# Optimization experiments

Hardware: AMD Instinct MI355X
Metric: run time of the kernel (lower is better)

## Reference

```python
import jax, jax.numpy as jnp
import numpy as np

B, N, M, K = 4, 16384, 16384, 16   # batch, points, centers, neighbors
C, O, G = 64, 64, 8                # in_planes, out_planes, group


def setup_inputs() -> dict:
    key = jax.random.key(0)
    ks = jax.random.split(key, 16)
    r = lambda i, sh, s=1.0: jax.random.normal(ks[i], sh, jnp.float32) * s
    return dict(
        center_pos=r(0, (B, M, 3)),
        center_fea=r(1, (B, C, M)),
        pos=r(2, (B, N, 3)),
        fea=r(3, (B, C, N)),
        idx=jax.random.randint(ks[4], (B, M, K), 0, N, jnp.int32),
        # linear q/k/v
        Wq=r(5, (C, O), 0.05), bq=jnp.zeros((O,), jnp.float32),
        Wk=r(6, (C, O), 0.05), bk=jnp.zeros((O,), jnp.float32),
        Wv=r(7, (C, O), 0.05), bv=jnp.zeros((O,), jnp.float32),
        # center_pos_encode: conv1x1(3->O, no bias) + folded BN (scale,shift) + relu + conv1x1(O->O)
        cpe_w1=r(8, (3, O), 0.05), cpe_s=jnp.ones((O,), jnp.float32), cpe_b=jnp.zeros((O,), jnp.float32),
        cpe_w2=r(9, (O, O), 0.05), cpe_b2=jnp.zeros((O,), jnp.float32),
        # pos_encode (Conv2d 1x1 == per-point linear)
        pe_w1=r(10, (3, O), 0.05), pe_s=jnp.ones((O,), jnp.float32), pe_b=jnp.zeros((O,), jnp.float32),
        pe_w2=r(11, (O, O), 0.05), pe_b2=jnp.zeros((O,), jnp.float32),
        # weight_encode (O -> G)
        we_w1=r(12, (O, G), 0.05), we_s=jnp.ones((G,), jnp.float32), we_b=jnp.zeros((G,), jnp.float32),
        we_w2=r(13, (G, G), 0.05), we_b2=jnp.zeros((G,), jnp.float32),
    )


def _mlp2(x, w1, s, b, w2, b2):
    # conv1x1(no bias) -> inference BatchNorm folded to (scale, shift) -> ReLU -> conv1x1(+bias)
    h = jax.nn.relu(x @ w1 * s + b)
    return h @ w2 + b2


def reference(center_pos, center_fea, pos, fea, idx,
              Wq, bq, Wk, bk, Wv, bv,
              cpe_w1, cpe_s, cpe_b, cpe_w2, cpe_b2,
              pe_w1, pe_s, pe_b, pe_w2, pe_b2,
              we_w1, we_s, we_b, we_w2, we_b2):
    x_q = center_fea.transpose(0, 2, 1) @ Wq + bq        # [B,M,O]
    ft = fea.transpose(0, 2, 1)                          # [B,N,C]
    x_k = ft @ Wk + bk                                   # [B,N,O]
    x_v = ft @ Wv + bv                                   # [B,N,O]

    gather = jax.vmap(lambda a, i: a[i])                 # per-batch irregular gather
    nk = gather(x_k, idx)                                # [B,M,K,O]
    nv = gather(x_v, idx)                                # [B,M,K,O]
    npos = gather(pos, idx) - center_pos[:, :, None, :]  # [B,M,K,3] relative coords

    cpr = _mlp2(center_pos, cpe_w1, cpe_s, cpe_b, cpe_w2, cpe_b2)  # [B,M,O]
    pr = _mlp2(npos, pe_w1, pe_s, pe_b, pe_w2, pe_b2)              # [B,M,K,O]

    r_qk = nk - x_q[:, :, None, :] + cpr[:, :, None, :]  # [B,M,K,O]
    v = nv + pr                                          # [B,M,K,O]

    w = _mlp2(r_qk, we_w1, we_s, we_b, we_w2, we_b2)     # [B,M,K,G]
    w = jax.nn.softmax(w, axis=2)                        # softmax over neighbors

    v = v.reshape(B, M, K, G, O // G)
    out = jnp.einsum('bmkgi,bmkg->bmgi', v, w).reshape(B, M, O)
    return out.transpose(0, 2, 1)                        # [B,O,M]
```

## Files before the change

kernel.cpp:

```cpp
#include <hip/hip_runtime.h>
#include <hip/hip_bf16.h>

typedef unsigned short u16;
typedef __attribute__((ext_vector_type(8))) __bf16 bf8v;
typedef __attribute__((ext_vector_type(4))) float f32x4;
typedef __attribute__((ext_vector_type(4))) unsigned uint4v;

#define B_ 4
#define N_ 16384
#define M_ 16384
#define K_ 16
#define C_ 64
#define O_ 64
#define G_ 8

__device__ __forceinline__ float bf2f(u16 x){
  union { unsigned u; float f; } v; v.u = ((unsigned)x) << 16; return v.f;
}
__device__ __forceinline__ u16 f2bf(float f){
  union { float f; unsigned u; } v; v.f = f;
  unsigned u = v.u;
  return (u16)((u + 0x7FFFu + ((u >> 16) & 1u)) >> 16);
}
union pk2 { unsigned u; _Float16 h[2]; };
__device__ __forceinline__ unsigned packh(float a, float b){
  pk2 p; p.h[0] = (_Float16)a; p.h[1] = (_Float16)b; return p.u;
}

__global__ __launch_bounds__(256) void setup_kernel(
    const float* __restrict__ Wq, const float* __restrict__ bq,
    const float* __restrict__ cpe_w2, const float* __restrict__ cpe_b2,
    const float* __restrict__ we_w1,
    u16* __restrict__ bw, float* __restrict__ cinit)
{
  __shared__ float sWe[512];
  int tid = threadIdx.x;
  for (int e = tid; e < 512; e += 256) sWe[e] = we_w1[e];
  __syncthreads();
  int k = tid >> 1, g0 = (tid & 1)*4;
  const float* brow = (k < 64) ? (cpe_w2 + k*64) : (Wq + (k-64)*64);
  float sgn = (k < 64) ? 1.f : -1.f;
  float aw[4] = {0.f,0.f,0.f,0.f};
  for (int o = 0; o < 64; o++){
    float bo = brow[o]*sgn;
    #pragma unroll
    for (int gg=0; gg<4; gg++) aw[gg] += bo * sWe[o*8 + g0+gg];
  }
  #pragma unroll
  for (int gg=0; gg<4; gg++) bw[(g0+gg)*136 + k] = f2bf(aw[gg]);
  for (int e = tid; e < 2176; e += 256){
    int r = e / 136, cc = e % 136;
    if (r >= 8 || cc >= 128) bw[e] = 0;
  }
  if (tid < 8){
    float s = 0.f;
    for (int o = 0; o < 64; o++) s += (cpe_b2[o] - bq[o]) * sWe[o*8 + tid];
    cinit[tid] = s;
  }
}

__global__ __launch_bounds__(256) void pre_kernel(
    const float* __restrict__ center_pos, const float* __restrict__ center_fea,
    const float* __restrict__ fea,
    const float* __restrict__ Wk, const float* __restrict__ bk,
    const float* __restrict__ Wv, const float* __restrict__ bv,
    const float* __restrict__ cpe_w1, const float* __restrict__ cpe_s, const float* __restrict__ cpe_b,
    const u16* __restrict__ bw, const float* __restrict__ cinit,
    u16* __restrict__ xk, u16* __restrict__ xv, float* __restrict__ qw)
{
  __shared__ u16 sWT[128*72];
  __shared__ u16 sA[64*72];
  __shared__ u16 sOut[64*136];
  __shared__ float sMisc[256];
  int tid = threadIdx.x;
  int l = tid & 63, w = tid >> 6, c = l & 15, q = l >> 4;
  int blk = blockIdx.x;

  if (blk < 1024){
    int P0 = blk * 64; int b = P0 >> 14; int n0 = P0 & (N_-1);
    const float* fb = fea + (long)b*C_*N_;
    #pragma unroll
    for (int pp = 0; pp < 4; pp++){
      int k = pp*16 + (tid >> 4);
      int nf = (tid & 15)*4;
      f32x4 v = *(const f32x4*)&fb[(long)k*N_ + n0 + nf];
      sA[(nf+0)*72+k] = f2bf(v[0]); sA[(nf+1)*72+k] = f2bf(v[1]);
      sA[(nf+2)*72+k] = f2bf(v[2]); sA[(nf+3)*72+k] = f2bf(v[3]);
    }
    for (int e = tid; e < 8192; e += 256){
      int k = e >> 7, col = e & 127;
      float v = (col < 64) ? Wk[k*64 + col] : Wv[k*64 + (col-64)];
      sWT[col*72 + k] = f2bf(v);
    }
    if (tid < 128) sMisc[tid] = (tid < 64) ? bk[tid] : bv[tid-64];
    __syncthreads();

    bf8v af0 = *(const bf8v*)&sA[(w*16+c)*72 + q*8];
    bf8v af1 = *(const bf8v*)&sA[(w*16+c)*72 + 32 + q*8];

    f32x4 acc[8];
    #pragma unroll
    for (int t = 0; t < 8; t++){
      float bias = sMisc[16*t + c];
      f32x4 a_ = {bias, bias, bias, bias};
      bf8v b0 = *(const bf8v*)&sWT[(16*t + c)*72 + q*8];
      bf8v b1 = *(const bf8v*)&sWT[(16*t + c)*72 + 32 + q*8];
      a_ = __builtin_amdgcn_mfma_f32_16x16x32_bf16(af0, b0, a_, 0,0,0);
      a_ = __builtin_amdgcn_mfma_f32_16x16x32_bf16(af1, b1, a_, 0,0,0);
      acc[t] = a_;
    }
    #pragma unroll
    for (int t = 0; t < 8; t++)
      #pragma unroll
      for (int r = 0; r < 4; r++)
        sOut[(w*16 + q*4 + r)*136 + 16*t + c] = f2bf(acc[t][r]);
    __syncthreads();

    #pragma unroll
    for (int rep = 0; rep < 4; rep++){
      int chunk = rep*256 + tid;
      int pt = chunk >> 4, c8i = chunk & 15;
      uint4v val = *(const uint4v*)&sOut[pt*136 + c8i*8];
      int col8 = c8i*8;
      long row = (long)P0 + pt;
      if (col8 < 64) *(uint4v*)(xk + row*64 + col8)      = val;
      else           *(uint4v*)(xv + row*64 + (col8-64)) = val;
    }
  } else {
    int P0 = (blk - 1024) * 64; int b = P0 >> 14; int m0 = P0 & (M_-1);
    const float* cfb = center_fea + (long)b*C_*M_;
    float* sQ = (float*)sOut;
    #pragma unroll
    for (int pp = 0; pp < 4; pp++){
      int k = pp*16 + (tid >> 4);
      int nf = (tid & 15)*4;
      f32x4 v = *(const f32x4*)&cfb[(long)k*M_ + m0 + nf];
      sA[(nf+0)*72+k] = f2bf(v[0]); sA[(nf+1)*72+k] = f2bf(v[1]);
      sA[(nf+2)*72+k] = f2bf(v[2]); sA[(nf+3)*72+k] = f2bf(v[3]);
    }
    for (int e = tid; e < 2176; e += 256) sWT[e] = bw[e];
    if (tid < 64){
      float sc = cpe_s[tid];
      sMisc[tid]     = cpe_w1[tid]*sc;
      sMisc[64+tid]  = cpe_w1[64+tid]*sc;
      sMisc[128+tid] = cpe_w1[128+tid]*sc;
      sMisc[192+tid] = cpe_b[tid];
    }
    long c3 = (long)(P0 + w*16 + c)*3;
    float cp0 = center_pos[c3], cp1 = center_pos[c3+1], cp2 = center_pos[c3+2];
    __syncthreads();

    bf8v ah[2];
    #pragma unroll
    for (int ks = 0; ks < 2; ks++){
      union { bf8v v; u16 sv[8]; } ua;
      #pragma unroll
      for (int j = 0; j < 8; j++){
        int h = ks*32 + q*8 + j;
        float hv = cp0*sMisc[h] + cp1*sMisc[64+h] + cp2*sMisc[128+h] + sMisc[192+h];
        ua.sv[j] = f2bf(fmaxf(hv, 0.f));
      }
      ah[ks] = ua.v;
    }
    bf8v acf0 = *(const bf8v*)&sA[(w*16+c)*72 + q*8];
    bf8v acf1 = *(const bf8v*)&sA[(w*16+c)*72 + 32 + q*8];

    float ci = (c < 8) ? cinit[c] : 0.f;
    f32x4 aq = {ci, ci, ci, ci};
    {
      bf8v b0 = *(const bf8v*)&sWT[c*136 + q*8];
      bf8v b1 = *(const bf8v*)&sWT[c*136 + 32 + q*8];
      bf8v b2 = *(const bf8v*)&sWT[c*136 + 64 + q*8];
      bf8v b3 = *(const bf8v*)&sWT[c*136 + 96 + q*8];
      aq = __builtin_amdgcn_mfma_f32_16x16x32_bf16(ah[0], b0, aq, 0,0,0);
      aq = __builtin_amdgcn_mfma_f32_16x16x32_bf16(ah[1], b1, aq, 0,0,0);
      aq = __builtin_amdgcn_mfma_f32_16x16x32_bf16(acf0,  b2, aq, 0,0,0);
      aq = __builtin_amdgcn_mfma_f32_16x16x32_bf16(acf1,  b3, aq, 0,0,0);
    }
    __syncthreads();
    if (c < 8){
      #pragma unroll
      for (int r = 0; r < 4; r++) sQ[(w*16 + q*4 + r)*8 + c] = aq[r];
    }
    __syncthreads();
    for (int e = tid; e < 512; e += 256)
      qw[(long)P0*8 + e] = sQ[e];
  }
}

__global__ __launch_bounds__(256) void attn_kernel(
    const float* __restrict__ center_pos, const float* __restrict__ pos,
    const int* __restrict__ idx,
    const float* __restrict__ pe_w1, const float* __restrict__ pe_s, const float* __restrict__ pe_b,
    const float* __restrict__ pe_w2, const float* __restrict__ pe_b2,
    const float* __restrict__ we_w1, const float* __restrict__ we_s, const float* __restrict__ we_b,
    const float* __restrict__ we_w2, const float* __restrict__ we_b2,
    const u16* __restrict__ xk, const u16* __restrict__ xv, const float* __restrict__ qw,
    float* __restrict__ out)
{
  int tid = threadIdx.x;
  __shared__ float s_w1f[192], s_pb[64], s_pb2[64], s_ww2[64];
  __shared__ float s_ws8[8], s_wb8[8], s_wb28[8];
  __shared__ u16  s_stage[64*72 + 16*72];
  __shared__ u16  s_vt[4*2*16*72];
  __shared__ float s_tile[32*66];

  if (tid < 64){
    float sc = pe_s[tid];
    s_w1f[tid]     = pe_w1[tid]*sc;
    s_w1f[64+tid]  = pe_w1[64+tid]*sc;
    s_w1f[128+tid] = pe_w1[128+tid]*sc;
    s_pb[tid]  = pe_b[tid];
    s_pb2[tid] = pe_b2[tid];
    s_ww2[tid] = we_w2[tid];
  }
  if (tid >= 64 && tid < 72){
    int g = tid-64;
    s_ws8[g]=we_s[g]; s_wb8[g]=we_b[g]; s_wb28[g]=we_b2[g];
  }
  #pragma unroll
  for (int pp = 0; pp < 4; pp++){
    int row = pp*16 + (tid >> 4);
    int colf = (tid & 15)*4;
    f32x4 v = *(const f32x4*)&pe_w2[row*64 + colf];
    s_stage[(colf+0)*72+row] = f2bf(v[0]); s_stage[(colf+1)*72+row] = f2bf(v[1]);
    s_stage[(colf+2)*72+row] = f2bf(v[2]); s_stage[(colf+3)*72+row] = f2bf(v[3]);
  }
  u16* s2 = s_stage + 64*72;
  for (int e = tid; e < 512; e += 256){
    int k = e >> 3, cc = e & 7;
    s2[cc*72 + k] = f2bf(we_w1[e]);
  }
  for (int e = tid; e < 576; e += 256) s2[576 + e] = 0;
  __syncthreads();

  int w = tid >> 6, l = tid & 63, c = l & 15, q = l >> 4, c8 = c & 7, qb = l & 48;

  bf8v pw2f[4][2], ww1f[2];
  #pragma unroll
  for (int t = 0; t < 4; t++){
    pw2f[t][0] = *(const bf8v*)&s_stage[(t*16+c)*72 + q*8];
    pw2f[t][1] = *(const bf8v*)&s_stage[(t*16+c)*72 + 32 + q*8];
  }
  ww1f[0] = *(const bf8v*)&s2[c*72 + q*8];
  ww1f[1] = *(const bf8v*)&s2[c*72 + 32 + q*8];

  float ws_c = s_ws8[c8], wb_c = s_wb8[c8], wb2_c = s_wb28[c8];
  float w2col[8];
  #pragma unroll
  for (int g = 0; g < 8; g++) w2col[g] = s_ww2[g*8 + c8];
  float pb2t[4];
  #pragma unroll
  for (int t = 0; t < 4; t++) pb2t[t] = s_pb2[t*16 + c];

  int pbase = blockIdx.x * 32;
  int b = pbase >> 14;
  long xkb = (long)b * N_ * 64;
  u16* vt0 = s_vt + w*(2*16*72);
  u16* vt1 = vt0 + 16*72;
  int ch = c >> 3;

  int pb0 = pbase + w*8;
  int iv0 = idx[(long)pb0*16 + c];
  int iv1 = idx[(long)(pb0+1)*16 + c];
  float qp0 = qw[(long)pb0*8 + c8];
  float qp1 = qw[(long)(pb0+1)*8 + c8];
  long c30 = (long)pb0*3, c31 = (long)(pb0+1)*3;
  float cpA0 = center_pos[c30], cpA1 = center_pos[c30+1], cpA2 = center_pos[c30+2];
  float cpB0 = center_pos[c31], cpB1 = center_pos[c31+1], cpB2 = center_pos[c31+2];

  #pragma unroll 1
  for (int i = 0; i < 4; i++){
    long prA = ((long)b*N_ + iv0)*3, prB = ((long)b*N_ + iv1)*3;
    float pxA = pos[prA], pyA = pos[prA+1], pzA = pos[prA+2];
    float pxB = pos[prB], pyB = pos[prB+1], pzB = pos[prB+2];
    const u16* kr0 = xk + xkb + (long)iv0*64;
    const u16* kr1 = xk + xkb + (long)iv1*64;
    bf8v ka00 = *(const bf8v*)(kr0 + q*8),  ka01 = *(const bf8v*)(kr0 + 32 + q*8);
    bf8v ka10 = *(const bf8v*)(kr1 + q*8),  ka11 = *(const bf8v*)(kr1 + 32 + q*8);
    const u16* vr0 = xv + xkb + (long)iv0*64;
    const u16* vr1 = xv + xkb + (long)iv1*64;
    uint4v va00 = *(const uint4v*)(vr0 + q*8), va01 = *(const uint4v*)(vr0 + 32 + q*8);
    uint4v va10 = *(const uint4v*)(vr1 + q*8), va11 = *(const uint4v*)(vr1 + 32 + q*8);

    int p2 = pb0 + ((i < 3) ? 2*i + 2 : 2*i);
    int p3 = p2 + 1;
    int ivn0 = idx[(long)p2*16 + c];
    int ivn1 = idx[(long)p3*16 + c];
    float qpn0 = qw[(long)p2*8 + c8];
    float qpn1 = qw[(long)p3*8 + c8];
    long c3n0 = (long)p2*3, c3n1 = (long)p3*3;
    float cpnA0 = center_pos[c3n0], cpnA1 = center_pos[c3n0+1], cpnA2 = center_pos[c3n0+2];
    float cpnB0 = center_pos[c3n1], cpnB1 = center_pos[c3n1+1], cpnB2 = center_pos[c3n1+2];

    *(uint4v*)&vt0[c*72 + q*8]      = va00;
    *(uint4v*)&vt0[c*72 + 32 + q*8] = va01;
    *(uint4v*)&vt1[c*72 + q*8]      = va10;
    *(uint4v*)&vt1[c*72 + 32 + q*8] = va11;

    float npA0 = pxA - cpA0, npA1 = pyA - cpA1, npA2 = pzA - cpA2;
    float npB0 = pxB - cpB0, npB1 = pyB - cpB1, npB2 = pzB - cpB2;
    bf8v h1A[2], h1B[2];
    #pragma unroll
    for (int ks = 0; ks < 2; ks++){
      union { bf8v v; u16 s[8]; } ha, hb;
      #pragma unroll
      for (int j = 0; j < 8; j++){
        int o = ks*32 + q*8 + j;
        float w1 = s_w1f[o], w2 = s_w1f[64+o], w3 = s_w1f[128+o], bb = s_pb[o];
        ha.s[j] = f2bf(fmaxf(npA0*w1 + npA1*w2 + npA2*w3 + bb, 0.f));
        hb.s[j] = f2bf(fmaxf(npB0*w1 + npB1*w2 + npB2*w3 + bb, 0.f));
      }
      h1A[ks] = ha.v; h1B[ks] = hb.v;
    }

    f32x4 h2a0 = {qp0, qp0, qp0, qp0};
    f32x4 h2a1 = {qp1, qp1, qp1, qp1};
    h2a0 = __builtin_amdgcn_mfma_f32_16x16x32_bf16(ka00, ww1f[0], h2a0, 0,0,0);
    h2a1 = __builtin_amdgcn_mfma_f32_16x16x32_bf16(ka10, ww1f[0], h2a1, 0,0,0);
    h2a0 = __builtin_amdgcn_mfma_f32_16x16x32_bf16(ka01, ww1f[1], h2a0, 0,0,0);
    h2a1 = __builtin_amdgcn_mfma_f32_16x16x32_bf16(ka11, ww1f[1], h2a1, 0,0,0);

    float h2r0[4], h2r1[4];
    #pragma unroll
    for (int r = 0; r < 4; r++){
      h2r0[r] = fmaxf(h2a0[r]*ws_c + wb_c, 0.f);
      h2r1[r] = fmaxf(h2a1[r]*ws_c + wb_c, 0.f);
    }
    unsigned hp00 = packh(h2r0[0], h2r0[1]), hp01 = packh(h2r0[2], h2r0[3]);
    unsigned hp10 = packh(h2r1[0], h2r1[1]), hp11 = packh(h2r1[2], h2r1[3]);
    float wl0[4] = {wb2_c, wb2_c, wb2_c, wb2_c};
    float wl1[4] = {wb2_c, wb2_c, wb2_c, wb2_c};
    #pragma unroll
    for (int g = 0; g < 8; g++){
      float wg = w2col[g];
      pk2 a0; a0.u = (unsigned)__shfl((int)hp00, qb | g, 64);
      pk2 a1; a1.u = (unsigned)__shfl((int)hp01, qb | g, 64);
      pk2 b0; b0.u = (unsigned)__shfl((int)hp10, qb | g, 64);
      pk2 b1; b1.u = (unsigned)__shfl((int)hp11, qb | g, 64);
      wl0[0] += (float)a0.h[0]*wg; wl0[1] += (float)a0.h[1]*wg;
      wl0[2] += (float)a1.h[0]*wg; wl0[3] += (float)a1.h[1]*wg;
      wl1[0] += (float)b0.h[0]*wg; wl1[1] += (float)b0.h[1]*wg;
      wl1[2] += (float)b1.h[0]*wg; wl1[3] += (float)b1.h[1]*wg;
    }
    float e0[4], e1[4];
    #pragma unroll
    for (int r = 0; r < 4; r++){
      e0[r] = exp2f(wl0[r]*1.44269504f);
      e1[r] = exp2f(wl1[r]*1.44269504f);
    }
    float sm0 = e0[0]+e0[1]+e0[2]+e0[3];
    float sm1 = e1[0]+e1[1]+e1[2]+e1[3];
    sm0 += __shfl_xor(sm0, 16, 64); sm1 += __shfl_xor(sm1, 16, 64);
    sm0 += __shfl_xor(sm0, 32, 64); sm1 += __shfl_xor(sm1, 32, 64);
    float rn0 = 1.0f/sm0, rn1 = 1.0f/sm1;
    #pragma unroll
    for (int r = 0; r < 4; r++){ e0[r] *= rn0; e1[r] *= rn1; }
    unsigned ep00 = packh(e0[0], e0[1]), ep01 = packh(e0[2], e0[3]);
    unsigned ep10 = packh(e1[0], e1[1]), ep11 = packh(e1[2], e1[3]);

    float ov0[4], ov1[4];
    #pragma unroll
    for (int t = 0; t < 4; t++){
      f32x4 z0 = {0.f,0.f,0.f,0.f}, z1 = {0.f,0.f,0.f,0.f};
      z0 = __builtin_amdgcn_mfma_f32_16x16x32_bf16(h1A[0], pw2f[t][0], z0, 0,0,0);
      z1 = __builtin_amdgcn_mfma_f32_16x16x32_bf16(h1B[0], pw2f[t][0], z1, 0,0,0);
      z0 = __builtin_amdgcn_mfma_f32_16x16x32_bf16(h1A[1], pw2f[t][1], z0, 0,0,0);
      z1 = __builtin_amdgcn_mfma_f32_16x16x32_bf16(h1B[1], pw2f[t][1], z1, 0,0,0);
      int src = qb | (t*2 + ch);
      pk2 wA0; wA0.u = (unsigned)__shfl((int)ep00, src, 64);
      pk2 wA1; wA1.u = (unsigned)__shfl((int)ep01, src, 64);
      pk2 wB0; wB0.u = (unsigned)__shfl((int)ep10, src, 64);
      pk2 wB1; wB1.u = (unsigned)__shfl((int)ep11, src, 64);
      float a = 0.f, bacc = 0.f;
      a += (z0[0] + bf2f(vt0[(q*4+0)*72 + t*16 + c])) * (float)wA0.h[0];
      a += (z0[1] + bf2f(vt0[(q*4+1)*72 + t*16 + c])) * (float)wA0.h[1];
      a += (z0[2] + bf2f(vt0[(q*4+2)*72 + t*16 + c])) * (float)wA1.h[0];
      a += (z0[3] + bf2f(vt0[(q*4+3)*72 + t*16 + c])) * (float)wA1.h[1];
      bacc += (z1[0] + bf2f(vt1[(q*4+0)*72 + t*16 + c])) * (float)wB0.h[0];
      bacc += (z1[1] + bf2f(vt1[(q*4+1)*72 + t*16 + c])) * (float)wB0.h[1];
      bacc += (z1[2] + bf2f(vt1[(q*4+2)*72 + t*16 + c])) * (float)wB1.h[0];
      bacc += (z1[3] + bf2f(vt1[(q*4+3)*72 + t*16 + c])) * (float)wB1.h[1];
      ov0[t] = a; ov1[t] = bacc;
    }
    #pragma unroll
    for (int t = 0; t < 4; t++){
      ov0[t] += __shfl_xor(ov0[t], 16, 64);
      ov1[t] += __shfl_xor(ov1[t], 16, 64);
      ov0[t] += __shfl_xor(ov0[t], 32, 64);
      ov1[t] += __shfl_xor(ov1[t], 32, 64);
      ov0[t] += pb2t[t]; ov1[t] += pb2t[t];
    }
    float s0 = ov0[0], s1 = ov1[0];
    s0 = (q==1) ? ov0[1] : s0;  s1 = (q==1) ? ov1[1] : s1;
    s0 = (q==2) ? ov0[2] : s0;  s1 = (q==2) ? ov1[2] : s1;
    s0 = (q==3) ? ov0[3] : s0;  s1 = (q==3) ? ov1[3] : s1;
    s_tile[(w*8 + 2*i + 0)*66 + l] = s0;
    s_tile[(w*8 + 2*i + 1)*66 + l] = s1;

    iv0 = ivn0; iv1 = ivn1; qp0 = qpn0; qp1 = qpn1;
    cpA0 = cpnA0; cpA1 = cpnA1; cpA2 = cpnA2;
    cpB0 = cpnB0; cpB1 = cpnB1; cpB2 = cpnB2;
  }
  __syncthreads();

  int o0 = tid >> 5, pt = tid & 31;
  int m0 = pbase & (M_-1);
  long outb = ((long)b*64) * M_ + m0 + pt;
  #pragma unroll
  for (int ii = 0; ii < 8; ii++){
    int o = o0*8 + ii;
    out[outb + (long)o*M_] = s_tile[pt*66 + o];
  }
}

extern "C" void kernel_launch(void* const* d_in, const int* in_sizes, int n_in,
                              void* d_out, int out_size, void* d_ws, size_t ws_size,
                              hipStream_t stream) {
  const float* center_pos = (const float*)d_in[0];
  const float* center_fea = (const float*)d_in[1];
  const float* pos        = (const float*)d_in[2];
  const float* fea        = (const float*)d_in[3];
  const int*   idx        = (const int*)d_in[4];
  const float* Wq = (const float*)d_in[5];   const float* bq = (const float*)d_in[6];
  const float* Wk = (const float*)d_in[7];   const float* bk = (const float*)d_in[8];
  const float* Wv = (const float*)d_in[9];   const float* bv = (const float*)d_in[10];
  const float* cpe_w1 = (const float*)d_in[11]; const float* cpe_s = (const float*)d_in[12];
  const float* cpe_b  = (const float*)d_in[13]; const float* cpe_w2 = (const float*)d_in[14];
  const float* cpe_b2 = (const float*)d_in[15];
  const float* pe_w1 = (const float*)d_in[16]; const float* pe_s = (const float*)d_in[17];
  const float* pe_b  = (const float*)d_in[18]; const float* pe_w2 = (const float*)d_in[19];
  const float* pe_b2 = (const float*)d_in[20];
  const float* we_w1 = (const float*)d_in[21]; const float* we_s = (const float*)d_in[22];
  const float* we_b  = (const float*)d_in[23]; const float* we_w2 = (const float*)d_in[24];
  const float* we_b2 = (const float*)d_in[25];

  const size_t SZ = (size_t)B_*N_*64;
  u16* xk = (u16*)d_ws;
  u16* xv = xk + SZ;
  float* qwp = (float*)(xv + SZ);
  u16* bwp = (u16*)(qwp + (size_t)B_*M_*8);
  float* cinitp = (float*)(bwp + 2176);
  float* outp = (float*)d_out;

  hipLaunchKernelGGL(setup_kernel, dim3(1), dim3(256), 0, stream,
      Wq, bq, cpe_w2, cpe_b2, we_w1, bwp, cinitp);
  hipLaunchKernelGGL(pre_kernel, dim3(2048), dim3(256), 0, stream,
      center_pos, center_fea, fea, Wk, bk, Wv, bv,
      cpe_w1, cpe_s, cpe_b, bwp, cinitp, xk, xv, qwp);
  hipLaunchKernelGGL(attn_kernel, dim3(2048), dim3(256), 0, stream,
      center_pos, pos, idx, pe_w1, pe_s, pe_b, pe_w2, pe_b2,
      we_w1, we_s, we_b, we_w2, we_b2, xk, xv, qwp, outp);
}
```

Measured before the change: 224.7 us.

## Prepack K/V weights in setup, persist pre blocks, restructure attention per-point loop

```diff
diff --git a/kernel.cpp b/kernel.cpp
--- a/kernel.cpp
+++ b/kernel.cpp
@@ -31,23 +31,29 @@
     const float* __restrict__ Wq, const float* __restrict__ bq,
     const float* __restrict__ cpe_w2, const float* __restrict__ cpe_b2,
     const float* __restrict__ we_w1,
-    u16* __restrict__ bw, float* __restrict__ cinit)
+    const float* __restrict__ Wk, const float* __restrict__ bk,
+    const float* __restrict__ Wv, const float* __restrict__ bv,
+    const float* __restrict__ cpe_w1, const float* __restrict__ cpe_s, const float* __restrict__ cpe_b,
+    u16* __restrict__ bw, float* __restrict__ cinit,
+    u16* __restrict__ wkv, float* __restrict__ bias, float* __restrict__ cpe)
 {
   __shared__ float sWe[512];
   int tid = threadIdx.x;
   for (int e = tid; e < 512; e += 256) sWe[e] = we_w1[e];
   __syncthreads();
-  int k = tid >> 1, g0 = (tid & 1)*4;
-  const float* brow = (k < 64) ? (cpe_w2 + k*64) : (Wq + (k-64)*64);
-  float sgn = (k < 64) ? 1.f : -1.f;
-  float aw[4] = {0.f,0.f,0.f,0.f};
-  for (int o = 0; o < 64; o++){
-    float bo = brow[o]*sgn;
+  {
+    int k = tid >> 1, g0 = (tid & 1)*4;
+    const float* brow = (k < 64) ? (cpe_w2 + k*64) : (Wq + (k-64)*64);
+    float sgn = (k < 64) ? 1.f : -1.f;
+    float aw[4] = {0.f,0.f,0.f,0.f};
+    for (int o = 0; o < 64; o++){
+      float bo = brow[o]*sgn;
+      #pragma unroll
+      for (int gg=0; gg<4; gg++) aw[gg] += bo * sWe[o*8 + g0+gg];
+    }
     #pragma unroll
-    for (int gg=0; gg<4; gg++) aw[gg] += bo * sWe[o*8 + g0+gg];
-  }
-  #pragma unroll
-  for (int gg=0; gg<4; gg++) bw[(g0+gg)*136 + k] = f2bf(aw[gg]);
+    for (int gg=0; gg<4; gg++) bw[(g0+gg)*136 + k] = f2bf(aw[gg]);
+  }
   for (int e = tid; e < 2176; e += 256){
     int r = e / 136, cc = e % 136;
     if (r >= 8 || cc >= 128) bw[e] = 0;
@@ -57,15 +63,27 @@
     for (int o = 0; o < 64; o++) s += (cpe_b2[o] - bq[o]) * sWe[o*8 + tid];
     cinit[tid] = s;
   }
+  for (int e = tid; e < 9216; e += 256){
+    int col = e / 72, k = e - col*72;
+    float v = 0.f;
+    if (k < 64) v = (col < 64) ? Wk[k*64 + col] : Wv[k*64 + (col-64)];
+    wkv[e] = f2bf(v);
+  }
+  if (tid < 128) bias[tid] = (tid < 64) ? bk[tid] : bv[tid-64];
+  if (tid < 64){
+    float sc = cpe_s[tid];
+    cpe[tid]      = cpe_w1[tid]*sc;
+    cpe[64+tid]   = cpe_w1[64+tid]*sc;
+    cpe[128+tid]  = cpe_w1[128+tid]*sc;
+    cpe[192+tid]  = cpe_b[tid];
+  }
 }
 
 __global__ __launch_bounds__(256) void pre_kernel(
     const float* __restrict__ center_pos, const float* __restrict__ center_fea,
     const float* __restrict__ fea,
-    const float* __restrict__ Wk, const float* __restrict__ bk,
-    const float* __restrict__ Wv, const float* __restrict__ bv,
-    const float* __restrict__ cpe_w1, const float* __restrict__ cpe_s, const float* __restrict__ cpe_b,
     const u16* __restrict__ bw, const float* __restrict__ cinit,
+    const u16* __restrict__ wkv, const float* __restrict__ bias, const float* __restrict__ cpe,
     u16* __restrict__ xk, u16* __restrict__ xv, float* __restrict__ qw)
 {
   __shared__ u16 sWT[128*72];
@@ -76,115 +94,118 @@
   int l = tid & 63, w = tid >> 6, c = l & 15, q = l >> 4;
   int blk = blockIdx.x;
 
-  if (blk < 1024){
-    int P0 = blk * 64; int b = P0 >> 14; int n0 = P0 & (N_-1);
+  if (blk < 256){
+    int P0 = blk * 256; int b = P0 >> 14; int n00 = P0 & (N_-1);
     const float* fb = fea + (long)b*C_*N_;
-    #pragma unroll
-    for (int pp = 0; pp < 4; pp++){
-      int k = pp*16 + (tid >> 4);
-      int nf = (tid & 15)*4;
-      f32x4 v = *(const f32x4*)&fb[(long)k*N_ + n0 + nf];
-      sA[(nf+0)*72+k] = f2bf(v[0]); sA[(nf+1)*72+k] = f2bf(v[1]);
-      sA[(nf+2)*72+k] = f2bf(v[2]); sA[(nf+3)*72+k] = f2bf(v[3]);
-    }
-    for (int e = tid; e < 8192; e += 256){
-      int k = e >> 7, col = e & 127;
-      float v = (col < 64) ? Wk[k*64 + col] : Wv[k*64 + (col-64)];
-      sWT[col*72 + k] = f2bf(v);
-    }
-    if (tid < 128) sMisc[tid] = (tid < 64) ? bk[tid] : bv[tid-64];
-    __syncthreads();
-
-    bf8v af0 = *(const bf8v*)&sA[(w*16+c)*72 + q*8];
-    bf8v af1 = *(const bf8v*)&sA[(w*16+c)*72 + 32 + q*8];
-
-    f32x4 acc[8];
-    #pragma unroll
-    for (int t = 0; t < 8; t++){
-      float bias = sMisc[16*t + c];
-      f32x4 a_ = {bias, bias, bias, bias};
-      bf8v b0 = *(const bf8v*)&sWT[(16*t + c)*72 + q*8];
-      bf8v b1 = *(const bf8v*)&sWT[(16*t + c)*72 + 32 + q*8];
-      a_ = __builtin_amdgcn_mfma_f32_16x16x32_bf16(af0, b0, a_, 0,0,0);
-      a_ = __builtin_amdgcn_mfma_f32_16x16x32_bf16(af1, b1, a_, 0,0,0);
-      acc[t] = a_;
-    }
-    #pragma unroll
-    for (int t = 0; t < 8; t++)
-      #pragma unroll
-      for (int r = 0; r < 4; r++)
-        sOut[(w*16 + q*4 + r)*136 + 16*t + c] = f2bf(acc[t][r]);
-    __syncthreads();
-
-    #pragma unroll
-    for (int rep = 0; rep < 4; rep++){
-      int chunk = rep*256 + tid;
-      int pt = chunk >> 4, c8i = chunk & 15;
-      uint4v val = *(const uint4v*)&sOut[pt*136 + c8i*8];
-      int col8 = c8i*8;
-      long row = (long)P0 + pt;
-      if (col8 < 64) *(uint4v*)(xk + row*64 + col8)      = val;
-      else           *(uint4v*)(xv + row*64 + (col8-64)) = val;
+    for (int e = tid; e < 1152; e += 256)
+      ((uint4v*)sWT)[e] = ((const uint4v*)wkv)[e];
+    if (tid < 128) sMisc[tid] = bias[tid];
+
+    #pragma unroll 1
+    for (int s = 0; s < 4; s++){
+      int n0 = n00 + s*64;
+      #pragma unroll
+      for (int pp = 0; pp < 4; pp++){
+        int k = pp*16 + (tid >> 4);
+        int nf = (tid & 15)*4;
+        f32x4 v = *(const f32x4*)&fb[(long)k*N_ + n0 + nf];
+        sA[(nf+0)*72+k] = f2bf(v[0]); sA[(nf+1)*72+k] = f2bf(v[1]);
+        sA[(nf+2)*72+k] = f2bf(v[2]); sA[(nf+3)*72+k] = f2bf(v[3]);
+      }
+      __syncthreads();
+
+      bf8v af0 = *(const bf8v*)&sA[(w*16+c)*72 + q*8];
+      bf8v af1 = *(const bf8v*)&sA[(w*16+c)*72 + 32 + q*8];
+      f32x4 acc[8];
+      #pragma unroll
+      for (int t = 0; t < 8; t++){
+        float bb = sMisc[16*t + c];
+        f32x4 a_ = {bb, bb, bb, bb};
+        bf8v b0 = *(const bf8v*)&sWT[(16*t + c)*72 + q*8];
+        bf8v b1 = *(const bf8v*)&sWT[(16*t + c)*72 + 32 + q*8];
+        a_ = __builtin_amdgcn_mfma_f32_16x16x32_bf16(af0, b0, a_, 0,0,0);
+        a_ = __builtin_amdgcn_mfma_f32_16x16x32_bf16(af1, b1, a_, 0,0,0);
+        acc[t] = a_;
+      }
+      #pragma unroll
+      for (int t = 0; t < 8; t++)
+        #pragma unroll
+        for (int r = 0; r < 4; r++)
+          sOut[(w*16 + q*4 + r)*136 + 16*t + c] = f2bf(acc[t][r]);
+      __syncthreads();
+
+      #pragma unroll
+      for (int rep = 0; rep < 4; rep++){
+        int chunk = rep*256 + tid;
+        int pt = chunk >> 4, c8i = chunk & 15;
+        uint4v val = *(const uint4v*)&sOut[pt*136 + c8i*8];
+        int col8 = c8i*8;
+        long row = (long)P0 + s*64 + pt;
+        if (col8 < 64) *(uint4v*)(xk + row*64 + col8)      = val;
+        else           *(uint4v*)(xv + row*64 + (col8-64)) = val;
+      }
+      __syncthreads();
     }
   } else {
-    int P0 = (blk - 1024) * 64; int b = P0 >> 14; int m0 = P0 & (M_-1);
+    int P0 = (blk - 256) * 256; int b = P0 >> 14; int m00 = P0 & (M_-1);
     const float* cfb = center_fea + (long)b*C_*M_;
     float* sQ = (float*)sOut;
-    #pragma unroll
-    for (int pp = 0; pp < 4; pp++){
-      int k = pp*16 + (tid >> 4);
-      int nf = (tid & 15)*4;
-      f32x4 v = *(const f32x4*)&cfb[(long)k*M_ + m0 + nf];
-      sA[(nf+0)*72+k] = f2bf(v[0]); sA[(nf+1)*72+k] = f2bf(v[1]);
-      sA[(nf+2)*72+k] = f2bf(v[2]); sA[(nf+3)*72+k] = f2bf(v[3]);
-    }
-    for (int e = tid; e < 2176; e += 256) sWT[e] = bw[e];
-    if (tid < 64){
-      float sc = cpe_s[tid];
-      sMisc[tid]     = cpe_w1[tid]*sc;
-      sMisc[64+tid]  = cpe_w1[64+tid]*sc;
-      sMisc[128+tid] = cpe_w1[128+tid]*sc;
-      sMisc[192+tid] = cpe_b[tid];
-    }
-    long c3 = (long)(P0 + w*16 + c)*3;
-    float cp0 = center_pos[c3], cp1 = center_pos[c3+1], cp2 = center_pos[c3+2];
-    __syncthreads();
-
-    bf8v ah[2];
-    #pragma unroll
-    for (int ks = 0; ks < 2; ks++){
-      union { bf8v v; u16 sv[8]; } ua;
-      #pragma unroll
-      for (int j = 0; j < 8; j++){
-        int h = ks*32 + q*8 + j;
-        float hv = cp0*sMisc[h] + cp1*sMisc[64+h] + cp2*sMisc[128+h] + sMisc[192+h];
-        ua.sv[j] = f2bf(fmaxf(hv, 0.f));
-      }
-      ah[ks] = ua.v;
-    }
-    bf8v acf0 = *(const bf8v*)&sA[(w*16+c)*72 + q*8];
-    bf8v acf1 = *(const bf8v*)&sA[(w*16+c)*72 + 32 + q*8];
-
-    float ci = (c < 8) ? cinit[c] : 0.f;
-    f32x4 aq = {ci, ci, ci, ci};
-    {
-      bf8v b0 = *(const bf8v*)&sWT[c*136 + q*8];
-      bf8v b1 = *(const bf8v*)&sWT[c*136 + 32 + q*8];
-      bf8v b2 = *(const bf8v*)&sWT[c*136 + 64 + q*8];
-      bf8v b3 = *(const bf8v*)&sWT[c*136 + 96 + q*8];
-      aq = __builtin_amdgcn_mfma_f32_16x16x32_bf16(ah[0], b0, aq, 0,0,0);
-      aq = __builtin_amdgcn_mfma_f32_16x16x32_bf16(ah[1], b1, aq, 0,0,0);
-      aq = __builtin_amdgcn_mfma_f32_16x16x32_bf16(acf0,  b2, aq, 0,0,0);
-      aq = __builtin_amdgcn_mfma_f32_16x16x32_bf16(acf1,  b3, aq, 0,0,0);
-    }
-    __syncthreads();
-    if (c < 8){
-      #pragma unroll
-      for (int r = 0; r < 4; r++) sQ[(w*16 + q*4 + r)*8 + c] = aq[r];
-    }
-    __syncthreads();
-    for (int e = tid; e < 512; e += 256)
-      qw[(long)P0*8 + e] = sQ[e];
+    for (int e = tid; e < 272; e += 256)
+      ((uint4v*)sWT)[e] = ((const uint4v*)bw)[e];
+    if (tid < 256) sMisc[tid] = cpe[tid];
+
+    #pragma unroll 1
+    for (int s = 0; s < 4; s++){
+      int m0 = m00 + s*64;
+      #pragma unroll
+      for (int pp = 0; pp < 4; pp++){
+        int k = pp*16 + (tid >> 4);
+        int nf = (tid & 15)*4;
+        f32x4 v = *(const f32x4*)&cfb[(long)k*M_ + m0 + nf];
+        sA[(nf+0)*72+k] = f2bf(v[0]); sA[(nf+1)*72+k] = f2bf(v[1]);
+        sA[(nf+2)*72+k] = f2bf(v[2]); sA[(nf+3)*72+k] = f2bf(v[3]);
+      }
+      long c3 = (long)(P0 + s*64 + w*16 + c)*3;
+      float cp0 = center_pos[c3], cp1 = center_pos[c3+1], cp2 = center_pos[c3+2];
+      __syncthreads();
+
+      bf8v ah[2];
+      #pragma unroll
+      for (int ks = 0; ks < 2; ks++){
+        union { bf8v v; u16 sv[8]; } ua;
+        #pragma unroll
+        for (int j = 0; j < 8; j++){
+          int h = ks*32 + q*8 + j;
+          float hv = cp0*sMisc[h] + cp1*sMisc[64+h] + cp2*sMisc[128+h] + sMisc[192+h];
+          ua.sv[j] = f2bf(fmaxf(hv, 0.f));
+        }
+        ah[ks] = ua.v;
+      }
+      bf8v acf0 = *(const bf8v*)&sA[(w*16+c)*72 + q*8];
+      bf8v acf1 = *(const bf8v*)&sA[(w*16+c)*72 + 32 + q*8];
+
+      float ci = (c < 8) ? cinit[c] : 0.f;
+      f32x4 aq = {ci, ci, ci, ci};
+      {
+        bf8v b0 = *(const bf8v*)&sWT[c*136 + q*8];
+        bf8v b1 = *(const bf8v*)&sWT[c*136 + 32 + q*8];
+        bf8v b2 = *(const bf8v*)&sWT[c*136 + 64 + q*8];
+        bf8v b3 = *(const bf8v*)&sWT[c*136 + 96 + q*8];
+        aq = __builtin_amdgcn_mfma_f32_16x16x32_bf16(ah[0], b0, aq, 0,0,0);
+        aq = __builtin_amdgcn_mfma_f32_16x16x32_bf16(ah[1], b1, aq, 0,0,0);
+        aq = __builtin_amdgcn_mfma_f32_16x16x32_bf16(acf0,  b2, aq, 0,0,0);
+        aq = __builtin_amdgcn_mfma_f32_16x16x32_bf16(acf1,  b3, aq, 0,0,0);
+      }
+      __syncthreads();
+      if (c < 8){
+        #pragma unroll
+        for (int r = 0; r < 4; r++) sQ[(w*16 + q*4 + r)*8 + c] = aq[r];
+      }
+      __syncthreads();
+      for (int e = tid; e < 512; e += 256)
+        qw[(long)(P0 + s*64)*8 + e] = sQ[e];
+      __syncthreads();
+    }
   }
 }
 
@@ -201,9 +222,10 @@
   int tid = threadIdx.x;
   __shared__ float s_w1f[192], s_pb[64], s_pb2[64], s_ww2[64];
   __shared__ float s_ws8[8], s_wb8[8], s_wb28[8];
-  __shared__ u16  s_stage[64*72 + 16*72];
-  __shared__ u16  s_vt[4*2*16*72];
+  __shared__ f32x4 s_dyn4[1232];
   __shared__ float s_tile[32*66];
+
+  char* dynb = (char*)s_dyn4;
 
   if (tid < 64){
     float sc = pe_s[tid];
@@ -218,189 +240,186 @@
     int g = tid-64;
     s_ws8[g]=we_s[g]; s_wb8[g]=we_b[g]; s_wb28[g]=we_b2[g];
   }
+  u16* stg = (u16*)dynb;
   #pragma unroll
   for (int pp = 0; pp < 4; pp++){
     int row = pp*16 + (tid >> 4);
     int colf = (tid & 15)*4;
     f32x4 v = *(const f32x4*)&pe_w2[row*64 + colf];
-    s_stage[(colf+0)*72+row] = f2bf(v[0]); s_stage[(colf+1)*72+row] = f2bf(v[1]);
-    s_stage[(colf+2)*72+row] = f2bf(v[2]); s_stage[(colf+3)*72+row] = f2bf(v[3]);
-  }
-  u16* s2 = s_stage + 64*72;
+    stg[(colf+0)*72+row] = f2bf(v[0]); stg[(colf+1)*72+row] = f2bf(v[1]);
+    stg[(colf+2)*72+row] = f2bf(v[2]); stg[(colf+3)*72+row] = f2bf(v[3]);
+  }
+  u16* stg2 = (u16*)(dynb + 9216);
   for (int e = tid; e < 512; e += 256){
     int k = e >> 3, cc = e & 7;
-    s2[cc*72 + k] = f2bf(we_w1[e]);
-  }
-  for (int e = tid; e < 576; e += 256) s2[576 + e] = 0;
+    stg2[cc*72 + k] = f2bf(we_w1[e]);
+  }
+  for (int e = tid; e < 576; e += 256) stg2[576 + e] = 0;
   __syncthreads();
 
   int w = tid >> 6, l = tid & 63, c = l & 15, q = l >> 4, c8 = c & 7, qb = l & 48;
 
-  bf8v pw2f[4][2], ww1f[2];
+  bf8v pw2f[4][2], ww1f[2], w2B;
   #pragma unroll
   for (int t = 0; t < 4; t++){
-    pw2f[t][0] = *(const bf8v*)&s_stage[(t*16+c)*72 + q*8];
-    pw2f[t][1] = *(const bf8v*)&s_stage[(t*16+c)*72 + 32 + q*8];
-  }
-  ww1f[0] = *(const bf8v*)&s2[c*72 + q*8];
-  ww1f[1] = *(const bf8v*)&s2[c*72 + 32 + q*8];
-
+    pw2f[t][0] = *(const bf8v*)&stg[(t*16+c)*72 + q*8];
+    pw2f[t][1] = *(const bf8v*)&stg[(t*16+c)*72 + 32 + q*8];
+  }
+  ww1f[0] = *(const bf8v*)&stg2[c*72 + q*8];
+  ww1f[1] = *(const bf8v*)&stg2[c*72 + 32 + q*8];
+  {
+    union { bf8v v; u16 s[8]; } uu;
+    #pragma unroll
+    for (int j = 0; j < 8; j++)
+      uu.s[j] = (q == 0 && c < 8) ? f2bf(s_ww2[j*8 + c]) : (u16)0;
+    w2B = uu.v;
+  }
   float ws_c = s_ws8[c8], wb_c = s_wb8[c8], wb2_c = s_wb28[c8];
-  float w2col[8];
-  #pragma unroll
-  for (int g = 0; g < 8; g++) w2col[g] = s_ww2[g*8 + c8];
-  float pb2t[4];
-  #pragma unroll
-  for (int t = 0; t < 4; t++) pb2t[t] = s_pb2[t*16 + c];
+  float pb2l = s_pb2[l];
+  __syncthreads();
+
+  float* sv  = (float*)(dynb + w*4928);
+  u16*  swt  = (u16*) (dynb + w*4928 + 4352);
+  u16*  sh   = (u16*) (dynb + w*4928 + 4672);
 
   int pbase = blockIdx.x * 32;
   int b = pbase >> 14;
   long xkb = (long)b * N_ * 64;
-  u16* vt0 = s_vt + w*(2*16*72);
-  u16* vt1 = vt0 + 16*72;
   int ch = c >> 3;
-
-  int pb0 = pbase + w*8;
-  int iv0 = idx[(long)pb0*16 + c];
-  int iv1 = idx[(long)(pb0+1)*16 + c];
-  float qp0 = qw[(long)pb0*8 + c8];
-  float qp1 = qw[(long)(pb0+1)*8 + c8];
-  long c30 = (long)pb0*3, c31 = (long)(pb0+1)*3;
-  float cpA0 = center_pos[c30], cpA1 = center_pos[c30+1], cpA2 = center_pos[c30+2];
-  float cpB0 = center_pos[c31], cpB1 = center_pos[c31+1], cpB2 = center_pos[c31+2];
+  int gl = (l >> 3) & 7;
+
+  int p = pbase + w*8;
+  int iv = idx[(long)p*16 + c];
+  float qpv = qw[(long)p*8 + c8];
+  long c30 = (long)p*3;
+  float cp0 = center_pos[c30], cp1 = center_pos[c30+1], cp2 = center_pos[c30+2];
+  long pr30 = ((long)b*N_ + iv) * 3;
+  float px = pos[pr30], py = pos[pr30+1], pz = pos[pr30+2];
+  const u16* krow0 = xk + xkb + (long)iv * 64;
+  bf8v ka0 = *(const bf8v*)(krow0 + q*8);
+  bf8v ka1 = *(const bf8v*)(krow0 + 32 + q*8);
+  const u16* vrow0 = xv + xkb + (long)iv * 64;
+  uint4v va0 = *(const uint4v*)(vrow0 + q*8);
+  uint4v va1 = *(const uint4v*)(vrow0 + 32 + q*8);
 
   #pragma unroll 1
-  for (int i = 0; i < 4; i++){
-    long prA = ((long)b*N_ + iv0)*3, prB = ((long)b*N_ + iv1)*3;
-    float pxA = pos[prA], pyA = pos[prA+1], pzA = pos[prA+2];
-    float pxB = pos[prB], pyB = pos[prB+1], pzB = pos[prB+2];
-    const u16* kr0 = xk + xkb + (long)iv0*64;
-    const u16* kr1 = xk + xkb + (long)iv1*64;
-    bf8v ka00 = *(const bf8v*)(kr0 + q*8),  ka01 = *(const bf8v*)(kr0 + 32 + q*8);
-    bf8v ka10 = *(const bf8v*)(kr1 + q*8),  ka11 = *(const bf8v*)(kr1 + 32 + q*8);
-    const u16* vr0 = xv + xkb + (long)iv0*64;
-    const u16* vr1 = xv + xkb + (long)iv1*64;
-    uint4v va00 = *(const uint4v*)(vr0 + q*8), va01 = *(const uint4v*)(vr0 + 32 + q*8);
-    uint4v va10 = *(const uint4v*)(vr1 + q*8), va11 = *(const uint4v*)(vr1 + 32 + q*8);
-
-    int p2 = pb0 + ((i < 3) ? 2*i + 2 : 2*i);
-    int p3 = p2 + 1;
-    int ivn0 = idx[(long)p2*16 + c];
-    int ivn1 = idx[(long)p3*16 + c];
-    float qpn0 = qw[(long)p2*8 + c8];
-    float qpn1 = qw[(long)p3*8 + c8];
-    long c3n0 = (long)p2*3, c3n1 = (long)p3*3;
-    float cpnA0 = center_pos[c3n0], cpnA1 = center_pos[c3n0+1], cpnA2 = center_pos[c3n0+2];
-    float cpnB0 = center_pos[c3n1], cpnB1 = center_pos[c3n1+1], cpnB2 = center_pos[c3n1+2];
-
-    *(uint4v*)&vt0[c*72 + q*8]      = va00;
-    *(uint4v*)&vt0[c*72 + 32 + q*8] = va01;
-    *(uint4v*)&vt1[c*72 + q*8]      = va10;
-    *(uint4v*)&vt1[c*72 + 32 + q*8] = va11;
-
-    float npA0 = pxA - cpA0, npA1 = pyA - cpA1, npA2 = pzA - cpA2;
-    float npB0 = pxB - cpB0, npB1 = pyB - cpB1, npB2 = pzB - cpB2;
-    bf8v h1A[2], h1B[2];
+  for (int i = 0; i < 8; i++){
+    int pn = p + ((i < 7) ? 1 : 0);
+    int iv_n = idx[(long)pn*16 + c];
+    float qpv_n = qw[(long)pn*8 + c8];
+    long c3n = (long)pn*3;
+    float cpn0 = center_pos[c3n], cpn1 = center_pos[c3n+1], cpn2 = center_pos[c3n+2];
+    long pr3n = ((long)b*N_ + iv_n) * 3;
+    float pxn = pos[pr3n], pyn = pos[pr3n+1], pzn = pos[pr3n+2];
+    const u16* krn = xk + xkb + (long)iv_n * 64;
+    bf8v kan0 = *(const bf8v*)(krn + q*8);
+    bf8v kan1 = *(const bf8v*)(krn + 32 + q*8);
+    const u16* vrn = xv + xkb + (long)iv_n * 64;
+    uint4v van0 = *(const uint4v*)(vrn + q*8);
+    uint4v van1 = *(const uint4v*)(vrn + 32 + q*8);
+
+    {
+      union { uint4v u; u16 s[8]; } A0, A1;
+      A0.u = va0; A1.u = va1;
+      f32x4 vf0, vf1, vf2, vf3;
+      #pragma unroll
+      for (int jj = 0; jj < 4; jj++){
+        vf0[jj] = bf2f(A0.s[jj]);   vf1[jj] = bf2f(A0.s[4+jj]);
+        vf2[jj] = bf2f(A1.s[jj]);   vf3[jj] = bf2f(A1.s[4+jj]);
+      }
+      f32x4* d0 = (f32x4*)&sv[c*68 + q*8];
+      d0[0] = vf0; d0[1] = vf1;
+      f32x4* d1 = (f32x4*)&sv[c*68 + 32 + q*8];
+      d1[0] = vf2; d1[1] = vf3;
+    }
+
+    float np0 = px - cp0, np1 = py - cp1, np2 = pz - cp2;
+    bf8v h1f[2];
     #pragma unroll
     for (int ks = 0; ks < 2; ks++){
-      union { bf8v v; u16 s[8]; } ha, hb;
+      union { bf8v v; u16 s[8]; } hu;
       #pragma unroll
       for (int j = 0; j < 8; j++){
         int o = ks*32 + q*8 + j;
-        float w1 = s_w1f[o], w2 = s_w1f[64+o], w3 = s_w1f[128+o], bb = s_pb[o];
-        ha.s[j] = f2bf(fmaxf(npA0*w1 + npA1*w2 + npA2*w3 + bb, 0.f));
-        hb.s[j] = f2bf(fmaxf(npB0*w1 + npB1*w2 + npB2*w3 + bb, 0.f));
-      }
-      h1A[ks] = ha.v; h1B[ks] = hb.v;
-    }
-
-    f32x4 h2a0 = {qp0, qp0, qp0, qp0};
-    f32x4 h2a1 = {qp1, qp1, qp1, qp1};
-    h2a0 = __builtin_amdgcn_mfma_f32_16x16x32_bf16(ka00, ww1f[0], h2a0, 0,0,0);
-    h2a1 = __builtin_amdgcn_mfma_f32_16x16x32_bf16(ka10, ww1f[0], h2a1, 0,0,0);
-    h2a0 = __builtin_amdgcn_mfma_f32_16x16x32_bf16(ka01, ww1f[1], h2a0, 0,0,0);
-    h2a1 = __builtin_amdgcn_mfma_f32_16x16x32_bf16(ka11, ww1f[1], h2a1, 0,0,0);
-
-    float h2r0[4], h2r1[4];
-    #pragma unroll
-    for (int r = 0; r < 4; r++){
-      h2r0[r] = fmaxf(h2a0[r]*ws_c + wb_c, 0.f);
-      h2r1[r] = fmaxf(h2a1[r]*ws_c + wb_c, 0.f);
-    }
-    unsigned hp00 = packh(h2r0[0], h2r0[1]), hp01 = packh(h2r0[2], h2r0[3]);
-    unsigned hp10 = packh(h2r1[0], h2r1[1]), hp11 = packh(h2r1[2], h2r1[3]);
-    float wl0[4] = {wb2_c, wb2_c, wb2_c, wb2_c};
-    float wl1[4] = {wb2_c, wb2_c, wb2_c, wb2_c};
-    #pragma unroll
-    for (int g = 0; g < 8; g++){
-      float wg = w2col[g];
-      pk2 a0; a0.u = (unsigned)__shfl((int)hp00, qb | g, 64);
-      pk2 a1; a1.u = (unsigned)__shfl((int)hp01, qb | g, 64);
-      pk2 b0; b0.u = (unsigned)__shfl((int)hp10, qb | g, 64);
-      pk2 b1; b1.u = (unsigned)__shfl((int)hp11, qb | g, 64);
-      wl0[0] += (float)a0.h[0]*wg; wl0[1] += (float)a0.h[1]*wg;
-      wl0[2] += (float)a1.h[0]*wg; wl0[3] += (float)a1.h[1]*wg;
-      wl1[0] += (float)b0.h[0]*wg; wl1[1] += (float)b0.h[1]*wg;
-      wl1[2] += (float)b1.h[0]*wg; wl1[3] += (float)b1.h[1]*wg;
-    }
-    float e0[4], e1[4];
-    #pragma unroll
-    for (int r = 0; r < 4; r++){
-      e0[r] = exp2f(wl0[r]*1.44269504f);
-      e1[r] = exp2f(wl1[r]*1.44269504f);
-    }
-    float sm0 = e0[0]+e0[1]+e0[2]+e0[3];
-    float sm1 = e1[0]+e1[1]+e1[2]+e1[3];
-    sm0 += __shfl_xor(sm0, 16, 64); sm1 += __shfl_xor(sm1, 16, 64);
-    sm0 += __shfl_xor(sm0, 32, 64); sm1 += __shfl_xor(sm1, 32, 64);
-    float rn0 = 1.0f/sm0, rn1 = 1.0f/sm1;
-    #pragma unroll
-    for (int r = 0; r < 4; r++){ e0[r] *= rn0; e1[r] *= rn1; }
-    unsigned ep00 = packh(e0[0], e0[1]), ep01 = packh(e0[2], e0[3]);
-    unsigned ep10 = packh(e1[0], e1[1]), ep11 = packh(e1[2], e1[3]);
-
-    float ov0[4], ov1[4];
+        float hv = np0*s_w1f[o] + np1*s_w1f[64+o] + np2*s_w1f[128+o] + s_pb[o];
+        hu.s[j] = f2bf(fmaxf(hv, 0.f));
+      }
+      h1f[ks] = hu.v;
+    }
+
+    f32x4 h2a = {qpv, qpv, qpv, qpv};
+    h2a = __builtin_amdgcn_mfma_f32_16x16x32_bf16(ka0, ww1f[0], h2a, 0,0,0);
+    h2a = __builtin_amdgcn_mfma_f32_16x16x32_bf16(ka1, ww1f[1], h2a, 0,0,0);
+
+    if (c < 8){
+      #pragma unroll
+      for (int r = 0; r < 4; r++)
+        sh[(q*4+r)*8 + c] = f2bf(fmaxf(h2a[r]*ws_c + wb_c, 0.f));
+    }
+    bf8v hrow = *(const bf8v*)&sh[c*8];
+    bf8v zf; { union { bf8v v; u16 s[8]; } uz;
+      #pragma unroll
+      for (int j=0;j<8;j++) uz.s[j]=0; zf = uz.v; }
+    bf8v ahf = (q == 0) ? hrow : zf;
+
+    f32x4 wlv = {wb2_c, wb2_c, wb2_c, wb2_c};
+    wlv = __builtin_amdgcn_mfma_f32_16x16x32_bf16(ahf, w2B, wlv, 0,0,0);
+
+    float e0 = exp2f(wlv[0]*1.44269504f);
+    float e1 = exp2f(wlv[1]*1.44269504f);
+    float e2 = exp2f(wlv[2]*1.44269504f);
+    float e3 = exp2f(wlv[3]*1.44269504f);
+    float sm = e0+e1+e2+e3;
+    sm += __shfl_xor(sm, 16, 64);
+    sm += __shfl_xor(sm, 32, 64);
+    float rn = 1.0f / sm;
+    e0 *= rn; e1 *= rn; e2 *= rn; e3 *= rn;
+    unsigned ep0 = packh(e0, e1), ep1 = packh(e2, e3);
+
+    if (c < 8){
+      *(unsigned*)&swt[c*20 + q*4]     = ep0;
+      *(unsigned*)&swt[c*20 + q*4 + 2] = ep1;
+    }
+
+    float ov[4];
     #pragma unroll
     for (int t = 0; t < 4; t++){
-      f32x4 z0 = {0.f,0.f,0.f,0.f}, z1 = {0.f,0.f,0.f,0.f};
-      z0 = __builtin_amdgcn_mfma_f32_16x16x32_bf16(h1A[0], pw2f[t][0], z0, 0,0,0);
-      z1 = __builtin_amdgcn_mfma_f32_16x16x32_bf16(h1B[0], pw2f[t][0], z1, 0,0,0);
-      z0 = __builtin_amdgcn_mfma_f32_16x16x32_bf16(h1A[1], pw2f[t][1], z0, 0,0,0);
-      z1 = __builtin_amdgcn_mfma_f32_16x16x32_bf16(h1B[1], pw2f[t][1], z1, 0,0,0);
+      f32x4 z = {0.f,0.f,0.f,0.f};
+      z = __builtin_amdgcn_mfma_f32_16x16x32_bf16(h1f[0], pw2f[t][0], z, 0,0,0);
+      z = __builtin_amdgcn_mfma_f32_16x16x32_bf16(h1f[1], pw2f[t][1], z, 0,0,0);
       int src = qb | (t*2 + ch);
-      pk2 wA0; wA0.u = (unsigned)__shfl((int)ep00, src, 64);
-      pk2 wA1; wA1.u = (unsigned)__shfl((int)ep01, src, 64);
-      pk2 wB0; wB0.u = (unsigned)__shfl((int)ep10, src, 64);
-      pk2 wB1; wB1.u = (unsigned)__shfl((int)ep11, src, 64);
-      float a = 0.f, bacc = 0.f;
-      a += (z0[0] + bf2f(vt0[(q*4+0)*72 + t*16 + c])) * (float)wA0.h[0];
-      a += (z0[1] + bf2f(vt0[(q*4+1)*72 + t*16 + c])) * (float)wA0.h[1];
-      a += (z0[2] + bf2f(vt0[(q*4+2)*72 + t*16 + c])) * (float)wA1.h[0];
-      a += (z0[3] + bf2f(vt0[(q*4+3)*72 + t*16 + c])) * (float)wA1.h[1];
-      bacc += (z1[0] + bf2f(vt1[(q*4+0)*72 + t*16 + c])) * (float)wB0.h[0];
-      bacc += (z1[1] + bf2f(vt1[(q*4+1)*72 + t*16 + c])) * (float)wB0.h[1];
-      bacc += (z1[2] + bf2f(vt1[(q*4+2)*72 + t*16 + c])) * (float)wB1.h[0];
-      bacc += (z1[3] + bf2f(vt1[(q*4+3)*72 + t*16 + c])) * (float)wB1.h[1];
-      ov0[t] = a; ov1[t] = bacc;
+      pk2 wA; wA.u = (unsigned)__shfl((int)ep0, src, 64);
+      pk2 wB; wB.u = (unsigned)__shfl((int)ep1, src, 64);
+      ov[t] = z[0]*(float)wA.h[0] + z[1]*(float)wA.h[1]
+            + z[2]*(float)wB.h[0] + z[3]*(float)wB.h[1];
     }
     #pragma unroll
     for (int t = 0; t < 4; t++){
-      ov0[t] += __shfl_xor(ov0[t], 16, 64);
-      ov1[t] += __shfl_xor(ov1[t], 16, 64);
-      ov0[t] += __shfl_xor(ov0[t], 32, 64);
-      ov1[t] += __shfl_xor(ov1[t], 32, 64);
-      ov0[t] += pb2t[t]; ov1[t] += pb2t[t];
-    }
-    float s0 = ov0[0], s1 = ov1[0];
-    s0 = (q==1) ? ov0[1] : s0;  s1 = (q==1) ? ov1[1] : s1;
-    s0 = (q==2) ? ov0[2] : s0;  s1 = (q==2) ? ov1[2] : s1;
-    s0 = (q==3) ? ov0[3] : s0;  s1 = (q==3) ? ov1[3] : s1;
-    s_tile[(w*8 + 2*i + 0)*66 + l] = s0;
-    s_tile[(w*8 + 2*i + 1)*66 + l] = s1;
-
-    iv0 = ivn0; iv1 = ivn1; qp0 = qpn0; qp1 = qpn1;
-    cpA0 = cpnA0; cpA1 = cpnA1; cpA2 = cpnA2;
-    cpB0 = cpnB0; cpB1 = cpnB1; cpB2 = cpnB2;
+      ov[t] += __shfl_xor(ov[t], 16, 64);
+      ov[t] += __shfl_xor(ov[t], 32, 64);
+    }
+    float ovsel = ov[0];
+    ovsel = (q==1) ? ov[1] : ovsel;
+    ovsel = (q==2) ? ov[2] : ovsel;
+    ovsel = (q==3) ? ov[3] : ovsel;
+
+    float acc = 0.f;
+    {
+      const unsigned* wr = (const unsigned*)&swt[gl*20];
+      #pragma unroll
+      for (int k2 = 0; k2 < 8; k2++){
+        pk2 wp; wp.u = wr[k2];
+        acc += sv[(2*k2)*68 + l]   * (float)wp.h[0];
+        acc += sv[(2*k2+1)*68 + l] * (float)wp.h[1];
+      }
+    }
+
+    s_tile[(w*8+i)*66 + l] = ovsel + acc + pb2l;
+
+    p = pn; iv = iv_n; qpv = qpv_n;
+    cp0 = cpn0; cp1 = cpn1; cp2 = cpn2;
+    px = pxn; py = pyn; pz = pzn;
+    ka0 = kan0; ka1 = kan1; va0 = van0; va1 = van1;
   }
   __syncthreads();
 
@@ -441,13 +460,17 @@
   float* qwp = (float*)(xv + SZ);
   u16* bwp = (u16*)(qwp + (size_t)B_*M_*8);
   float* cinitp = (float*)(bwp + 2176);
+  u16* wkvp = (u16*)(cinitp + 8);
+  float* biasp = (float*)(wkvp + 9216);
+  float* cpep = biasp + 128;
   float* outp = (float*)d_out;
 
   hipLaunchKernelGGL(setup_kernel, dim3(1), dim3(256), 0, stream,
-      Wq, bq, cpe_w2, cpe_b2, we_w1, bwp, cinitp);
-  hipLaunchKernelGGL(pre_kernel, dim3(2048), dim3(256), 0, stream,
-      center_pos, center_fea, fea, Wk, bk, Wv, bv,
-      cpe_w1, cpe_s, cpe_b, bwp, cinitp, xk, xv, qwp);
+      Wq, bq, cpe_w2, cpe_b2, we_w1, Wk, bk, Wv, bv,
+      cpe_w1, cpe_s, cpe_b, bwp, cinitp, wkvp, biasp, cpep);
+  hipLaunchKernelGGL(pre_kernel, dim3(512), dim3(256), 0, stream,
+      center_pos, center_fea, fea, bwp, cinitp, wkvp, biasp, cpep,
+      xk, xv, qwp);
   hipLaunchKernelGGL(attn_kernel, dim3(2048), dim3(256), 0, stream,
       center_pos, pos, idx, pe_w1, pe_s, pe_b, pe_w2, pe_b2,
       we_w1, we_s, we_b, we_w2, we_b2, xk, xv, qwp, outp);
```

Result: no change. 229.1 us (+2.0%).
